# Kernel optimization log

Hardware: AMD Instinct MI355X
Metric: run time of the kernel (lower is better)

The kernel has to match this reference:

```python
import jax, jax.numpy as jnp
import numpy as np

EPS = 1e-5
H = 8  # num_heads


def _layernorm(x, g, b):
    m = x.mean(axis=-1, keepdims=True)
    v = jnp.mean((x - m) ** 2, axis=-1, keepdims=True)
    return (x - m) / jnp.sqrt(v + EPS) * g + b


def setup_inputs() -> dict:
    key = jax.random.key(0)
    ks = jax.random.split(key, 8)
    B, T, N, D, L = 4, 4096, 512, 1024, 768
    x = jax.random.normal(ks[0], (B, T, D), dtype=jnp.float32)
    cond = jax.random.normal(ks[1], (B, N, L), dtype=jnp.float32)
    # LayerNorm params
    ln_g = jnp.ones((D,), jnp.float32)
    ln_b = jnp.zeros((D,), jnp.float32)
    tln_g = jnp.ones((L,), jnp.float32)
    tln_b = jnp.zeros((L,), jnp.float32)
    # Linear params, stored as (in, out)
    Wq = jax.random.normal(ks[2], (D, D), jnp.float32) * 0.02
    bq = jnp.zeros((D,), jnp.float32)
    Wk = jax.random.normal(ks[3], (L, D), jnp.float32) * 0.02
    bk = jnp.zeros((D,), jnp.float32)
    Wv = jax.random.normal(ks[4], (L, D), jnp.float32) * 0.02
    bv = jnp.zeros((D,), jnp.float32)
    return {"input_tensor": x, "condition_tensor": cond,
            "ln_g": ln_g, "ln_b": ln_b, "tln_g": tln_g, "tln_b": tln_b,
            "Wq": Wq, "bq": bq, "Wk": Wk, "bk": bk, "Wv": Wv, "bv": bv}


def reference(input_tensor, condition_tensor, ln_g, ln_b, tln_g, tln_b,
              Wq, bq, Wk, bk, Wv, bv):
    B, T, D = input_tensor.shape
    N = condition_tensor.shape[1]
    xn = _layernorm(input_tensor, ln_g, ln_b)            # [B,T,D]
    cn = _layernorm(condition_tensor, tln_g, tln_b)      # [B,N,L]
    q = jnp.einsum('btd,de->bte', xn, Wq) + bq           # [B,T,D]
    k = jnp.einsum('bnl,ld->bnd', cn, Wk) + bk           # [B,N,D]
    v = jnp.einsum('bnl,ld->bnd', cn, Wv) + bv           # [B,N,D]
    q = jax.nn.softmax(q.reshape(B, T, H, D // H), axis=-1)  # softmax over head_dim
    k = jax.nn.softmax(k.reshape(B, N, H, D // H), axis=1)   # softmax over N
    v = v.reshape(B, N, H, D // H)
    context = jnp.einsum('bnhk,bnhv->bhkv', k, v)        # [B,H,hd,hd]
    y = jnp.einsum('bthk,bhkv->bthv', q, context).reshape(B, T, D)
    return y
```

## Files before the change

kernel.cpp:

```cpp
#include <hip/hip_runtime.h>
#include <hip/hip_bf16.h>
#include <stdint.h>

#define BATCH 4
#define TLEN  4096
#define DDIM  1024
#define NCOND 512
#define LDIM  768
#define NHEAD 8
#define HD    128

typedef __bf16 bf16x8 __attribute__((ext_vector_type(8)));
typedef float  f32x4  __attribute__((ext_vector_type(4)));

__device__ __forceinline__ unsigned short f2b(float f) {
    unsigned int u = __builtin_bit_cast(unsigned int, f);
    unsigned int r = (u + 0x7fffu + ((u >> 16) & 1u)) >> 16;
    return (unsigned short)r;
}
__device__ __forceinline__ float b2f(unsigned short s) {
    unsigned int u = ((unsigned int)s) << 16;
    return __builtin_bit_cast(float, u);
}

__device__ __forceinline__ void gl2lds(const void* g, void* l) {
    __builtin_amdgcn_global_load_lds(
        (const __attribute__((address_space(1))) void*)(uintptr_t)g,
        (__attribute__((address_space(3))) void*)(uintptr_t)l,
        16, 0, 0);
}

template<int NCH>
__global__ __launch_bounds__(256) void ln_apply(const float* __restrict__ x,
    const float* __restrict__ g, const float* __restrict__ bb,
    unsigned short* __restrict__ o, int rowlen)
{
    int wid = threadIdx.x >> 6, lane = threadIdx.x & 63;
    long r = (long)blockIdx.x * 4 + wid;
    const float* p = x + r * (long)rowlen;
    float4 v[NCH];
    float s = 0.f, ss = 0.f;
#pragma unroll
    for (int i = 0; i < NCH; i++) {
        v[i] = *(const float4*)(p + i * 256 + lane * 4);
        s  += v[i].x + v[i].y + v[i].z + v[i].w;
        ss += v[i].x * v[i].x + v[i].y * v[i].y + v[i].z * v[i].z + v[i].w * v[i].w;
    }
#pragma unroll
    for (int off = 32; off; off >>= 1) {
        s  += __shfl_xor(s,  off, 64);
        ss += __shfl_xor(ss, off, 64);
    }
    float mu = s / rowlen;
    float rs = rsqrtf(fmaxf(ss / rowlen - mu * mu, 0.f) + 1e-5f);
    unsigned short* po = o + r * (long)rowlen;
#pragma unroll
    for (int i = 0; i < NCH; i++) {
        int c = i * 256 + lane * 4;
        float4 gv = *(const float4*)(g + c);
        float4 bv = *(const float4*)(bb + c);
        ushort4 o4;
        o4.x = f2b((v[i].x - mu) * rs * gv.x + bv.x);
        o4.y = f2b((v[i].y - mu) * rs * gv.y + bv.y);
        o4.z = f2b((v[i].z - mu) * rs * gv.z + bv.z);
        o4.w = f2b((v[i].w - mu) * rs * gv.w + bv.w);
        *(ushort4*)(po + c) = o4;
    }
}

__global__ __launch_bounds__(256) void wtrans3(
    const float* __restrict__ Wq, const float* __restrict__ Wk,
    const float* __restrict__ Wv,
    unsigned short* __restrict__ wqT, unsigned short* __restrict__ wkvT)
{
    int z = blockIdx.z;
    int K = z ? LDIM : DDIM;
    int k0 = blockIdx.y * 32;
    if (k0 >= K) return;
    const float* W = z == 0 ? Wq : (z == 1 ? Wk : Wv);
    unsigned short* Wt = z == 0 ? wqT : (z == 1 ? wkvT : wkvT + 768 * 1024);

    __shared__ float t[32][33];
    int n0 = blockIdx.x * 32;
    int tx = threadIdx.x & 31, ty = threadIdx.x >> 5;
#pragma unroll
    for (int i = 0; i < 4; i++)
        t[ty + i * 8][tx] = W[(long)(k0 + ty + i * 8) * DDIM + n0 + tx];
    __syncthreads();
#pragma unroll
    for (int i = 0; i < 4; i++)
        Wt[(long)(n0 + ty + i * 8) * K + k0 + tx] = f2b(t[tx][ty + i * 8]);
}

__global__ __launch_bounds__(256) void gemm_kv(
    const unsigned short* __restrict__ A,
    const unsigned short* __restrict__ Bt,
    const float* __restrict__ bk, const float* __restrict__ bv,
    float* __restrict__ Ck,
    unsigned short* __restrict__ Cvv)
{
    int zi = blockIdx.z;
    const unsigned short* Bp = Bt + (long)zi * 1024 * LDIM;
    const float* bias = zi ? bv : bk;

    int m0 = blockIdx.y * 128, n0 = blockIdx.x * 128;
    int tid = threadIdx.x, lane = tid & 63, wid = tid >> 6;
    int l16 = lane & 15, quad = lane >> 4;
    int mw = (wid & 1) << 6, nw = (wid >> 1) << 6;

    __shared__ unsigned short sb[16384];

    f32x4 acc[4][4];
#pragma unroll
    for (int i = 0; i < 4; i++)
#pragma unroll
        for (int j = 0; j < 4; j++) { acc[i][j][0] = 0.f; acc[i][j][1] = 0.f; acc[i][j][2] = 0.f; acc[i][j][3] = 0.f; }

    int cg = (tid & 3) ^ ((tid >> 3) & 3);
    const unsigned short* ag = A  + (long)(m0 + (tid >> 2)) * LDIM + cg * 8;
    const unsigned short* bg = Bp + (long)(n0 + (tid >> 2)) * LDIM + cg * 8;
    const long a64 = 64L * LDIM;
    int wsl = wid * 512;
    int sw = (l16 >> 1) & 3;

    auto stage = [&](unsigned short* d, int ko) {
        gl2lds(ag + ko,        d + wsl);
        gl2lds(ag + a64 + ko,  d + wsl + 2048);
        gl2lds(bg + ko,        d + 4096 + wsl);
        gl2lds(bg + a64 + ko,  d + 4096 + wsl + 2048);
    };

    const int NT = LDIM >> 5;
    stage(sb, 0);
    stage(sb + 8192, 32);

    for (int t = 0; t < NT; ++t) {
        if (t + 1 < NT) asm volatile("s_waitcnt vmcnt(4)" ::: "memory");
        else            asm volatile("s_waitcnt vmcnt(0)" ::: "memory");
        __builtin_amdgcn_s_barrier();
        __builtin_amdgcn_sched_barrier(0);
        unsigned short* Ac = sb + (t & 1) * 8192;
        bf16x8 af[4], bfr[4];
#pragma unroll
        for (int i = 0; i < 4; i++)
            af[i] = *(const bf16x8*)&Ac[(mw + i * 16 + l16) * 32 + ((quad ^ sw) * 8)];
#pragma unroll
        for (int j = 0; j < 4; j++)
            bfr[j] = *(const bf16x8*)&Ac[4096 + (nw + j * 16 + l16) * 32 + ((quad ^ sw) * 8)];
#pragma unroll
        for (int i = 0; i < 4; i++)
#pragma unroll
            for (int j = 0; j < 4; j++)
                acc[i][j] = __builtin_amdgcn_mfma_f32_16x16x32_bf16(af[i], bfr[j], acc[i][j], 0, 0, 0);
        __builtin_amdgcn_s_barrier();
        __builtin_amdgcn_sched_barrier(0);
        if (t + 2 < NT) stage(Ac, (t + 2) << 5);
    }

#pragma unroll
    for (int j = 0; j < 4; j++) {
        int col = n0 + nw + j * 16 + l16;
        float bvv = bias[col];
#pragma unroll
        for (int i = 0; i < 4; i++) {
            int row0 = m0 + mw + i * 16 + (quad << 2);
#pragma unroll
            for (int r = 0; r < 4; r++) {
                float val = acc[i][j][r] + bvv;
                long idx = (long)(row0 + r) * DDIM + col;
                if (zi == 0) Ck[idx]  = val;
                else         Cvv[idx] = f2b(val);
            }
        }
    }
}

__global__ __launch_bounds__(256) void kstats(const float* __restrict__ k,
                                              float* __restrict__ Mv,
                                              float* __restrict__ Sv)
{
    int b = blockIdx.x >> 5, chunk = blockIdx.x & 31;
    int c = threadIdx.x & 31;
    int col = chunk * 32 + c;
    int ns  = threadIdx.x >> 5;
    const float* p = k + (long)b * NCOND * DDIM + col;
    float m = -1e30f, s = 0.f;
#pragma unroll 4
    for (int i = 0; i < 64; i++) {
        float v = p[(long)(ns * 64 + i) * DDIM];
        float nm = fmaxf(m, v);
        s = s * __expf(m - nm) + __expf(v - nm);
        m = nm;
    }
    __shared__ float shm[8][33], shs[8][33];
    shm[ns][c] = m; shs[ns][c] = s;
    __syncthreads();
    if (ns == 0) {
        float M = shm[0][c], S = shs[0][c];
#pragma unroll
        for (int t = 1; t < 8; t++) {
            float m2 = shm[t][c], s2 = shs[t][c];
            float nm = fmaxf(M, m2);
            S = S * __expf(M - nm) + s2 * __expf(m2 - nm);
            M = nm;
        }
        Mv[b * DDIM + col] = M;
        Sv[b * DDIM + col] = 1.f / S;
    }
}

__global__ __launch_bounds__(256) void ctx_mfma(const float* __restrict__ kraw,
    const unsigned short* __restrict__ v,
    const float* __restrict__ Mv, const float* __restrict__ Sv,
    float* __restrict__ ctxf)
{
    __shared__ unsigned short kT[128 * 72];
    __shared__ unsigned short vT[128 * 72];
    int s0 = blockIdx.x;
    int bh = blockIdx.y;
    int b = bh >> 3, h = bh & 7;
    int n0 = s0 * 64;
    int tid = threadIdx.x;

    const float* kp = kraw + (long)b * NCOND * DDIM + (long)n0 * DDIM + h * HD;
    const unsigned short* vp = v + (long)b * NCOND * DDIM + (long)n0 * DDIM + h * HD;
    const float* Mp = Mv + b * DDIM + h * HD;
    const float* Sp = Sv + b * DDIM + h * HD;

#pragma unroll 8
    for (int p = 0; p < 32; p++) {
        int e = p * 256 + tid;
        int nn = e >> 7, kk = e & 127;
        float val = __expf(kp[(long)nn * DDIM + kk] - Mp[kk]) * Sp[kk];
        kT[kk * 72 + nn] = f2b(val);
    }
#pragma unroll 8
    for (int p = 0; p < 16; p++) {
        int e = p * 256 + tid;
        int nn = e >> 6, v2 = (e & 63) * 2;
        unsigned int w = *(const unsigned int*)&vp[(long)nn * DDIM + v2];
        vT[v2 * 72 + nn]       = (unsigned short)w;
        vT[(v2 + 1) * 72 + nn] = (unsigned short)(w >> 16);
    }
    __syncthreads();

    int lane = tid & 63, wid = tid >> 6;
    int l16 = lane & 15, quad = lane >> 4;
    int mw = (wid & 1) << 6, nw = (wid >> 1) << 6;
    f32x4 acc[4][4];
#pragma unroll
    for (int i = 0; i < 4; i++)
#pragma unroll
        for (int j = 0; j < 4; j++) { acc[i][j][0] = 0.f; acc[i][j][1] = 0.f; acc[i][j][2] = 0.f; acc[i][j][3] = 0.f; }

#pragma unroll
    for (int ks = 0; ks < 2; ks++) {
        bf16x8 af[4], bfr[4];
#pragma unroll
        for (int i = 0; i < 4; i++)
            af[i] = *(const bf16x8*)&vT[(mw + i * 16 + l16) * 72 + ks * 32 + quad * 8];
#pragma unroll
        for (int j = 0; j < 4; j++)
            bfr[j] = *(const bf16x8*)&kT[(nw + j * 16 + l16) * 72 + ks * 32 + quad * 8];
#pragma unroll
        for (int i = 0; i < 4; i++)
#pragma unroll
            for (int j = 0; j < 4; j++)
                acc[i][j] = __builtin_amdgcn_mfma_f32_16x16x32_bf16(af[i], bfr[j], acc[i][j], 0, 0, 0);
    }

    float* cf = ctxf + ((long)bh << 14);
#pragma unroll
    for (int i = 0; i < 4; i++)
#pragma unroll
        for (int j = 0; j < 4; j++)
#pragma unroll
            for (int r = 0; r < 4; r++)
                atomicAdd(&cf[(mw + i * 16 + quad * 4 + r) * 128 + nw + j * 16 + l16],
                          acc[i][j][r]);
}

__global__ __launch_bounds__(256) void ctxcvt(const float* __restrict__ cf,
                                              unsigned short* __restrict__ ct)
{
    int i = (blockIdx.x * 256 + threadIdx.x) * 4;
    float4 v = *(const float4*)(cf + i);
    ushort4 o;
    o.x = f2b(v.x); o.y = f2b(v.y); o.z = f2b(v.z); o.w = f2b(v.w);
    *(ushort4*)(ct + i) = o;
}

__global__ __launch_bounds__(256, 4) void qfused(
    const unsigned short* __restrict__ xn,
    const unsigned short* __restrict__ wqT,
    const float* __restrict__ bq,
    const unsigned short* __restrict__ ctxT,
    float* __restrict__ out)
{
    __shared__ unsigned short buf[18432];
    unsigned short* Pb = buf;
    float* redM = (float*)(buf + 17408);
    float* redS = redM + 256;

    int head = blockIdx.y;
    int m0 = blockIdx.x * 128;
    int b  = m0 >> 12;
    int tid = threadIdx.x, lane = tid & 63, wid = tid >> 6;
    int l16 = lane & 15, quad = lane >> 4;
    int mw = (wid & 1) << 6, nw = (wid >> 1) << 6;
    int ch = wid >> 1;

    const unsigned short* cg2 = ctxT + ((long)(b * NHEAD + head) << 14);

    f32x4 acc[4][4];
#pragma unroll
    for (int i = 0; i < 4; i++)
#pragma unroll
        for (int j = 0; j < 4; j++) { acc[i][j][0] = 0.f; acc[i][j][1] = 0.f; acc[i][j][2] = 0.f; acc[i][j][3] = 0.f; }

    int cgs = (tid & 3) ^ ((tid >> 3) & 3);
    const unsigned short* ag = xn  + (long)(m0 + (tid >> 2)) * DDIM + cgs * 8;
    const unsigned short* bg = wqT + (long)(head * 128 + (tid >> 2)) * DDIM + cgs * 8;
    const long a64 = 64L * DDIM;
    int wsl = wid * 512;
    int sw = (l16 >> 1) & 3;

    auto stage = [&](unsigned short* d, int ko) {
        gl2lds(ag + ko,        d + wsl);
        gl2lds(ag + a64 + ko,  d + wsl + 2048);
        gl2lds(bg + ko,        d + 4096 + wsl);
        gl2lds(bg + a64 + ko,  d + 4096 + wsl + 2048);
    };

    const int NT = DDIM >> 5;
    stage(buf, 0);
    stage(buf + 8192, 32);

    for (int t = 0; t < NT; ++t) {
        if (t + 1 < NT) asm volatile("s_waitcnt vmcnt(4)" ::: "memory");
        else            asm volatile("s_waitcnt vmcnt(0)" ::: "memory");
        __builtin_amdgcn_s_barrier();
        __builtin_amdgcn_sched_barrier(0);
        unsigned short* Ac = buf + (t & 1) * 8192;
        bf16x8 af[4], bfr[4];
#pragma unroll
        for (int i = 0; i < 4; i++)
            af[i] = *(const bf16x8*)&Ac[(mw + i * 16 + l16) * 32 + ((quad ^ sw) * 8)];
#pragma unroll
        for (int j = 0; j < 4; j++)
            bfr[j] = *(const bf16x8*)&Ac[4096 + (nw + j * 16 + l16) * 32 + ((quad ^ sw) * 8)];
#pragma unroll
        for (int i = 0; i < 4; i++)
#pragma unroll
            for (int j = 0; j < 4; j++)
                acc[i][j] = __builtin_amdgcn_mfma_f32_16x16x32_bf16(af[i], bfr[j], acc[i][j], 0, 0, 0);
        __builtin_amdgcn_s_barrier();
        __builtin_amdgcn_sched_barrier(0);
        if (t + 2 < NT) stage(Ac, (t + 2) << 5);
    }

    float bvv[4];
#pragma unroll
    for (int j = 0; j < 4; j++) bvv[j] = bq[head * 128 + nw + j * 16 + l16];
#pragma unroll
    for (int i = 0; i < 4; i++)
#pragma unroll
        for (int j = 0; j < 4; j++)
#pragma unroll
            for (int r = 0; r < 4; r++) acc[i][j][r] += bvv[j];

    float mx[4][4];
#pragma unroll
    for (int i = 0; i < 4; i++)
#pragma unroll
        for (int r = 0; r < 4; r++) {
            float m = acc[i][0][r];
            m = fmaxf(m, acc[i][1][r]);
            m = fmaxf(m, acc[i][2][r]);
            m = fmaxf(m, acc[i][3][r]);
            mx[i][r] = m;
        }
#pragma unroll
    for (int off = 1; off < 16; off <<= 1)
#pragma unroll
        for (int i = 0; i < 4; i++)
#pragma unroll
            for (int r = 0; r < 4; r++)
                mx[i][r] = fmaxf(mx[i][r], __shfl_xor(mx[i][r], off, 64));
    if (l16 == 0) {
#pragma unroll
        for (int i = 0; i < 4; i++)
#pragma unroll
            for (int r = 0; r < 4; r++)
                redM[ch * 128 + mw + i * 16 + quad * 4 + r] = mx[i][r];
    }
    __syncthreads();

    float sm[4][4];
#pragma unroll
    for (int i = 0; i < 4; i++)
#pragma unroll
        for (int r = 0; r < 4; r++) {
            int row = mw + i * 16 + quad * 4 + r;
            float M = fmaxf(redM[row], redM[128 + row]);
            float s = 0.f;
#pragma unroll
            for (int j = 0; j < 4; j++) {
                unsigned short eb = f2b(__expf(acc[i][j][r] - M));
                Pb[row * 136 + nw + j * 16 + l16] = eb;
                s += b2f(eb);
            }
            sm[i][r] = s;
        }
#pragma unroll
    for (int off = 1; off < 16; off <<= 1)
#pragma unroll
        for (int i = 0; i < 4; i++)
#pragma unroll
            for (int r = 0; r < 4; r++)
                sm[i][r] += __shfl_xor(sm[i][r], off, 64);
    if (l16 == 0) {
#pragma unroll
        for (int i = 0; i < 4; i++)
#pragma unroll
            for (int r = 0; r < 4; r++)
                redS[ch * 128 + mw + i * 16 + quad * 4 + r] = sm[i][r];
    }
    __syncthreads();

    f32x4 acc2[4][4];
#pragma unroll
    for (int i = 0; i < 4; i++)
#pragma unroll
        for (int j = 0; j < 4; j++) { acc2[i][j][0] = 0.f; acc2[i][j][1] = 0.f; acc2[i][j][2] = 0.f; acc2[i][j][3] = 0.f; }
#pragma unroll
    for (int ks = 0; ks < 4; ks++) {
        bf16x8 af[4], bfr[4];
#pragma unroll
        for (int j = 0; j < 4; j++)
            bfr[j] = *(const bf16x8*)&cg2[(nw + j * 16 + l16) * 128 + ks * 32 + quad * 8];
#pragma unroll
        for (int i = 0; i < 4; i++)
            af[i] = *(const bf16x8*)&Pb[(mw + i * 16 + l16) * 136 + ks * 32 + quad * 8];
#pragma unroll
        for (int i = 0; i < 4; i++)
#pragma unroll
            for (int j = 0; j < 4; j++)
                acc2[i][j] = __builtin_amdgcn_mfma_f32_16x16x32_bf16(af[i], bfr[j], acc2[i][j], 0, 0, 0);
    }

#pragma unroll
    for (int i = 0; i < 4; i++)
#pragma unroll
        for (int r = 0; r < 4; r++) {
            int row = mw + i * 16 + quad * 4 + r;
            float invd = 1.f / (redS[row] + redS[128 + row]);
            float* op = out + (long)(m0 + row) * DDIM + head * 128;
#pragma unroll
            for (int j = 0; j < 4; j++)
                op[nw + j * 16 + l16] = acc2[i][j][r] * invd;
        }
}

extern "C" void kernel_launch(void* const* d_in, const int* in_sizes, int n_in,
                              void* d_out, int out_size, void* d_ws, size_t ws_size,
                              hipStream_t stream) {
    (void)in_sizes; (void)n_in; (void)out_size; (void)ws_size;
    const float* x     = (const float*)d_in[0];
    const float* cond  = (const float*)d_in[1];
    const float* ln_g  = (const float*)d_in[2];
    const float* ln_b  = (const float*)d_in[3];
    const float* tln_g = (const float*)d_in[4];
    const float* tln_b = (const float*)d_in[5];
    const float* Wq    = (const float*)d_in[6];
    const float* bq    = (const float*)d_in[7];
    const float* Wk    = (const float*)d_in[8];
    const float* bk    = (const float*)d_in[9];
    const float* Wv    = (const float*)d_in[10];
    const float* bv    = (const float*)d_in[11];
    float* out = (float*)d_out;

    uint8_t* w8 = (uint8_t*)d_ws;
    unsigned short* xn   = (unsigned short*)w8;
    unsigned short* cn   = (unsigned short*)(w8 + 33554432);
    unsigned short* wqT  = (unsigned short*)(w8 + 36700160);
    unsigned short* wkvT = (unsigned short*)(w8 + 38797312);
    float*          fk   = (float*)(w8 + 41943040);
    unsigned short* fvb  = (unsigned short*)(w8 + 50331648);
    float*          ctxf = (float*)(w8 + 54525952);
    unsigned short* ctxT = (unsigned short*)(w8 + 56623104);
    float*          Mv   = (float*)(w8 + 57671680);
    float*          Sv   = (float*)(w8 + 57688064);

    hipMemsetAsync(ctxf, 0, 32 * 128 * 128 * sizeof(float), stream);

    ln_apply<3><<<512, 256, 0, stream>>>(cond, tln_g, tln_b, cn, LDIM);
    ln_apply<4><<<4096, 256, 0, stream>>>(x, ln_g, ln_b, xn, DDIM);
    wtrans3<<<dim3(32, 32, 3), 256, 0, stream>>>(Wq, Wk, Wv, wqT, wkvT);

    gemm_kv<<<dim3(8, 16, 2), 256, 0, stream>>>(cn, wkvT, bk, bv, fk, fvb);

    kstats<<<128, 256, 0, stream>>>(fk, Mv, Sv);
    ctx_mfma<<<dim3(8, 32), 256, 0, stream>>>(fk, fvb, Mv, Sv, ctxf);
    ctxcvt<<<512, 256, 0, stream>>>(ctxf, ctxT);

    qfused<<<dim3(128, 8), 256, 0, stream>>>(xn, wqT, bq, ctxT, out);
}
```

Baseline: 254.7 us.

## Merge prep kernels, drop context atomics, and remap qfused blocks per XCD

Fuses the two LayerNorm launches and the weight transpose into a single prep kernel, which cuts launch overhead. The context kernel now loops over N inside each block instead of splitting N across blocks with fp32 atomics. That removes the memset, the atomics and the separate bf16 conversion kernel, at the cost of fewer blocks (128) with more serial work each. The qfused grid is flattened to 1D and remapped so that the eight heads of an m-tile land on the same XCD, which should improve L2 reuse of the xn rows.

After: 244.1 us. -4.2%, faster.

```diff
diff --git a/kernel.cpp b/kernel.cpp
--- a/kernel.cpp
+++ b/kernel.cpp
@@ -31,12 +31,11 @@
 }
 
 template<int NCH>
-__global__ __launch_bounds__(256) void ln_apply(const float* __restrict__ x,
+__device__ __forceinline__ void ln_row(const float* __restrict__ x,
     const float* __restrict__ g, const float* __restrict__ bb,
-    unsigned short* __restrict__ o, int rowlen)
+    unsigned short* __restrict__ o, long r, int lane)
 {
-    int wid = threadIdx.x >> 6, lane = threadIdx.x & 63;
-    long r = (long)blockIdx.x * 4 + wid;
+    const int rowlen = NCH * 256;
     const float* p = x + r * (long)rowlen;
     float4 v[NCH];
     float s = 0.f, ss = 0.f;
@@ -68,21 +67,34 @@
     }
 }
 
-__global__ __launch_bounds__(256) void wtrans3(
+__global__ __launch_bounds__(256) void prep(
+    const float* __restrict__ x, const float* __restrict__ ln_g,
+    const float* __restrict__ ln_b,
+    const float* __restrict__ cond, const float* __restrict__ tln_g,
+    const float* __restrict__ tln_b,
     const float* __restrict__ Wq, const float* __restrict__ Wk,
     const float* __restrict__ Wv,
+    unsigned short* __restrict__ xn, unsigned short* __restrict__ cn,
     unsigned short* __restrict__ wqT, unsigned short* __restrict__ wkvT)
 {
-    int z = blockIdx.z;
-    int K = z ? LDIM : DDIM;
-    int k0 = blockIdx.y * 32;
-    if (k0 >= K) return;
-    const float* W = z == 0 ? Wq : (z == 1 ? Wk : Wv);
-    unsigned short* Wt = z == 0 ? wqT : (z == 1 ? wkvT : wkvT + 768 * 1024);
-
+    int blk = blockIdx.x;
+    int tid = threadIdx.x, wid = tid >> 6, lane = tid & 63;
+    if (blk < 4096) {
+        ln_row<4>(x, ln_g, ln_b, xn, (long)blk * 4 + wid, lane);
+        return;
+    }
+    if (blk < 4608) {
+        ln_row<3>(cond, tln_g, tln_b, cn, (long)(blk - 4096) * 4 + wid, lane);
+        return;
+    }
+    int w = blk - 4608;
+    const float* W; unsigned short* Wt; int K, wi;
+    if (w < 1024)      { W = Wq; Wt = wqT;               K = DDIM; wi = w; }
+    else if (w < 1792) { W = Wk; Wt = wkvT;              K = LDIM; wi = w - 1024; }
+    else               { W = Wv; Wt = wkvT + 768 * 1024; K = LDIM; wi = w - 1792; }
+    int n0 = (wi & 31) * 32, k0 = (wi >> 5) * 32;
     __shared__ float t[32][33];
-    int n0 = blockIdx.x * 32;
-    int tx = threadIdx.x & 31, ty = threadIdx.x >> 5;
+    int tx = tid & 31, ty = tid >> 5;
 #pragma unroll
     for (int i = 0; i < 4; i++)
         t[ty + i * 8][tx] = W[(long)(k0 + ty + i * 8) * DDIM + n0 + tx];
@@ -209,85 +221,75 @@
     }
 }
 
-__global__ __launch_bounds__(256) void ctx_mfma(const float* __restrict__ kraw,
+__global__ __launch_bounds__(256) void ctx_mfma2(const float* __restrict__ kraw,
     const unsigned short* __restrict__ v,
     const float* __restrict__ Mv, const float* __restrict__ Sv,
-    float* __restrict__ ctxf)
+    unsigned short* __restrict__ ctxT)
 {
-    __shared__ unsigned short kT[128 * 72];
     __shared__ unsigned short vT[128 * 72];
-    int s0 = blockIdx.x;
-    int bh = blockIdx.y;
+    __shared__ unsigned short kT[32 * 72];
+    int kk0 = blockIdx.x * 32;
+    int bh  = blockIdx.y;
     int b = bh >> 3, h = bh & 7;
-    int n0 = s0 * 64;
-    int tid = threadIdx.x;
-
-    const float* kp = kraw + (long)b * NCOND * DDIM + (long)n0 * DDIM + h * HD;
-    const unsigned short* vp = v + (long)b * NCOND * DDIM + (long)n0 * DDIM + h * HD;
-    const float* Mp = Mv + b * DDIM + h * HD;
-    const float* Sp = Sv + b * DDIM + h * HD;
-
-#pragma unroll 8
-    for (int p = 0; p < 32; p++) {
-        int e = p * 256 + tid;
-        int nn = e >> 7, kk = e & 127;
-        float val = __expf(kp[(long)nn * DDIM + kk] - Mp[kk]) * Sp[kk];
-        kT[kk * 72 + nn] = f2b(val);
-    }
-#pragma unroll 8
-    for (int p = 0; p < 16; p++) {
-        int e = p * 256 + tid;
-        int nn = e >> 6, v2 = (e & 63) * 2;
-        unsigned int w = *(const unsigned int*)&vp[(long)nn * DDIM + v2];
-        vT[v2 * 72 + nn]       = (unsigned short)w;
-        vT[(v2 + 1) * 72 + nn] = (unsigned short)(w >> 16);
-    }
-    __syncthreads();
-
-    int lane = tid & 63, wid = tid >> 6;
+    int tid = threadIdx.x, lane = tid & 63, wid = tid >> 6;
     int l16 = lane & 15, quad = lane >> 4;
-    int mw = (wid & 1) << 6, nw = (wid >> 1) << 6;
-    f32x4 acc[4][4];
-#pragma unroll
-    for (int i = 0; i < 4; i++)
-#pragma unroll
-        for (int j = 0; j < 4; j++) { acc[i][j][0] = 0.f; acc[i][j][1] = 0.f; acc[i][j][2] = 0.f; acc[i][j][3] = 0.f; }
-
-#pragma unroll
-    for (int ks = 0; ks < 2; ks++) {
-        bf16x8 af[4], bfr[4];
-#pragma unroll
-        for (int i = 0; i < 4; i++)
-            af[i] = *(const bf16x8*)&vT[(mw + i * 16 + l16) * 72 + ks * 32 + quad * 8];
-#pragma unroll
-        for (int j = 0; j < 4; j++)
-            bfr[j] = *(const bf16x8*)&kT[(nw + j * 16 + l16) * 72 + ks * 32 + quad * 8];
-#pragma unroll
-        for (int i = 0; i < 4; i++)
-#pragma unroll
-            for (int j = 0; j < 4; j++)
-                acc[i][j] = __builtin_amdgcn_mfma_f32_16x16x32_bf16(af[i], bfr[j], acc[i][j], 0, 0, 0);
-    }
-
-    float* cf = ctxf + ((long)bh << 14);
-#pragma unroll
-    for (int i = 0; i < 4; i++)
-#pragma unroll
-        for (int j = 0; j < 4; j++)
+
+    const float* Mp = Mv + b * DDIM + h * HD + kk0;
+    const float* Sp = Sv + b * DDIM + h * HD + kk0;
+
+    f32x4 acc[2][2];
+#pragma unroll
+    for (int i = 0; i < 2; i++)
+#pragma unroll
+        for (int j = 0; j < 2; j++) { acc[i][j][0] = 0.f; acc[i][j][1] = 0.f; acc[i][j][2] = 0.f; acc[i][j][3] = 0.f; }
+
+    for (int s = 0; s < 8; s++) {
+        int n0 = s * 64;
+        const float* kp = kraw + (long)b * NCOND * DDIM + (long)n0 * DDIM + h * HD + kk0;
+        const unsigned short* vp = v + (long)b * NCOND * DDIM + (long)n0 * DDIM + h * HD;
+#pragma unroll
+        for (int p = 0; p < 8; p++) {
+            int e = p * 256 + tid;
+            int nn = e >> 5, kk = e & 31;
+            float val = __expf(kp[(long)nn * DDIM + kk] - Mp[kk]) * Sp[kk];
+            kT[kk * 72 + nn] = f2b(val);
+        }
+#pragma unroll
+        for (int p = 0; p < 16; p++) {
+            int e = p * 256 + tid;
+            int nn = e >> 6, v2 = (e & 63) * 2;
+            unsigned int w = *(const unsigned int*)&vp[(long)nn * DDIM + v2];
+            vT[v2 * 72 + nn]       = (unsigned short)w;
+            vT[(v2 + 1) * 72 + nn] = (unsigned short)(w >> 16);
+        }
+        __syncthreads();
+#pragma unroll
+        for (int ks = 0; ks < 2; ks++) {
+            bf16x8 af[2], bfr[2];
+#pragma unroll
+            for (int i = 0; i < 2; i++)
+                af[i] = *(const bf16x8*)&vT[(wid * 32 + i * 16 + l16) * 72 + ks * 32 + quad * 8];
+#pragma unroll
+            for (int j = 0; j < 2; j++)
+                bfr[j] = *(const bf16x8*)&kT[(j * 16 + l16) * 72 + ks * 32 + quad * 8];
+#pragma unroll
+            for (int i = 0; i < 2; i++)
+#pragma unroll
+                for (int j = 0; j < 2; j++)
+                    acc[i][j] = __builtin_amdgcn_mfma_f32_16x16x32_bf16(af[i], bfr[j], acc[i][j], 0, 0, 0);
+        }
+        __syncthreads();
+    }
+
+    unsigned short* cp = ctxT + ((long)bh << 14);
+#pragma unroll
+    for (int i = 0; i < 2; i++)
+#pragma unroll
+        for (int j = 0; j < 2; j++)
 #pragma unroll
             for (int r = 0; r < 4; r++)
-                atomicAdd(&cf[(mw + i * 16 + quad * 4 + r) * 128 + nw + j * 16 + l16],
-                          acc[i][j][r]);
-}
-
-__global__ __launch_bounds__(256) void ctxcvt(const float* __restrict__ cf,
-                                              unsigned short* __restrict__ ct)
-{
-    int i = (blockIdx.x * 256 + threadIdx.x) * 4;
-    float4 v = *(const float4*)(cf + i);
-    ushort4 o;
-    o.x = f2b(v.x); o.y = f2b(v.y); o.z = f2b(v.z); o.w = f2b(v.w);
-    *(ushort4*)(ct + i) = o;
+                cp[(wid * 32 + i * 16 + quad * 4 + r) * 128 + kk0 + j * 16 + l16] =
+                    f2b(acc[i][j][r]);
 }
 
 __global__ __launch_bounds__(256, 4) void qfused(
@@ -302,8 +304,11 @@
     float* redM = (float*)(buf + 17408);
     float* redS = redM + 256;
 
-    int head = blockIdx.y;
-    int m0 = blockIdx.x * 128;
+    int d = blockIdx.x;
+    int xcd = d & 7, slot = d >> 3;
+    int mtile = xcd * 16 + (slot >> 3);
+    int head = slot & 7;
+    int m0 = mtile * 128;
     int b  = m0 >> 12;
     int tid = threadIdx.x, lane = tid & 63, wid = tid >> 6;
     int l16 = lane & 15, quad = lane >> 4;
@@ -325,11 +330,11 @@
     int wsl = wid * 512;
     int sw = (l16 >> 1) & 3;
 
-    auto stage = [&](unsigned short* d, int ko) {
-        gl2lds(ag + ko,        d + wsl);
-        gl2lds(ag + a64 + ko,  d + wsl + 2048);
-        gl2lds(bg + ko,        d + 4096 + wsl);
-        gl2lds(bg + a64 + ko,  d + 4096 + wsl + 2048);
+    auto stage = [&](unsigned short* dst, int ko) {
+        gl2lds(ag + ko,        dst + wsl);
+        gl2lds(ag + a64 + ko,  dst + wsl + 2048);
+        gl2lds(bg + ko,        dst + 4096 + wsl);
+        gl2lds(bg + a64 + ko,  dst + 4096 + wsl + 2048);
     };
 
     const int NT = DDIM >> 5;
@@ -487,22 +492,14 @@
     unsigned short* wkvT = (unsigned short*)(w8 + 38797312);
     float*          fk   = (float*)(w8 + 41943040);
     unsigned short* fvb  = (unsigned short*)(w8 + 50331648);
-    float*          ctxf = (float*)(w8 + 54525952);
     unsigned short* ctxT = (unsigned short*)(w8 + 56623104);
     float*          Mv   = (float*)(w8 + 57671680);
     float*          Sv   = (float*)(w8 + 57688064);
 
-    hipMemsetAsync(ctxf, 0, 32 * 128 * 128 * sizeof(float), stream);
-
-    ln_apply<3><<<512, 256, 0, stream>>>(cond, tln_g, tln_b, cn, LDIM);
-    ln_apply<4><<<4096, 256, 0, stream>>>(x, ln_g, ln_b, xn, DDIM);
-    wtrans3<<<dim3(32, 32, 3), 256, 0, stream>>>(Wq, Wk, Wv, wqT, wkvT);
-
+    prep<<<7168, 256, 0, stream>>>(x, ln_g, ln_b, cond, tln_g, tln_b,
+                                   Wq, Wk, Wv, xn, cn, wqT, wkvT);
     gemm_kv<<<dim3(8, 16, 2), 256, 0, stream>>>(cn, wkvT, bk, bv, fk, fvb);
-
     kstats<<<128, 256, 0, stream>>>(fk, Mv, Sv);
-    ctx_mfma<<<dim3(8, 32), 256, 0, stream>>>(fk, fvb, Mv, Sv, ctxf);
-    ctxcvt<<<512, 256, 0, stream>>>(ctxf, ctxT);
-
-    qfused<<<dim3(128, 8), 256, 0, stream>>>(xn, wqT, bq, ctxT, out);
-}
+    ctx_mfma2<<<dim3(4, 32), 256, 0, stream>>>(fk, fvb, Mv, Sv, ctxT);
+    qfused<<<1024, 256, 0, stream>>>(xn, wqT, bq, ctxT, out);
+}
```
